# Kernel tuning notes

Measured on AMD Instinct MI355X. Metric: run time of the kernel, lower is better.

The kernel has to match this reference:

```python
import jax, jax.numpy as jnp
import numpy as np

B, T = 16384, 128  # batch, n_frames


def setup_inputs() -> dict:
    key = jax.random.key(0)
    k0, k1, k2, k3, k4, k5 = jax.random.split(key, 6)
    dir = jax.random.normal(k0, (B, 3), dtype=jnp.float32)
    R = jax.random.normal(k1, (B, T, 3, 3), dtype=jnp.float32)
    s = 1.0 / np.sqrt(3.0)  # torch LSTM default init scale (uniform +-1/sqrt(hidden))
    W_ih = jax.random.uniform(k2, (12, 3), jnp.float32, -s, s)
    W_hh = jax.random.uniform(k3, (12, 3), jnp.float32, -s, s)
    b_ih = jax.random.uniform(k4, (12,), jnp.float32, -s, s)
    b_hh = jax.random.uniform(k5, (12,), jnp.float32, -s, s)
    return {"dir": dir, "R": R, "W_ih": W_ih, "W_hh": W_hh, "b_ih": b_ih, "b_hh": b_hh}


def _rot_step(v, Rm):
    # v: [B,3], Rm: [B,3,3] -> Rm @ v
    nv = jnp.einsum('bij,bj->bi', Rm, v)
    return nv, nv


def _build_dirs(dir, R):
    n_frames = R.shape[1]
    half = n_frames // 2
    # Backward chain: dirs[i] = R[half-1-i]^T @ ... @ R[half-1]^T @ dir
    Rt_back = jnp.swapaxes(jnp.flip(R[:, :half], axis=1), 2, 3)  # [B, half, 3, 3]
    _, back = jax.lax.scan(_rot_step, dir, jnp.swapaxes(Rt_back, 0, 1))  # [half, B, 3]
    # Forward chain: dirs[i] = R[i-1] @ ... @ R[half] @ dir for i in half+1..n-1
    Rf = jnp.swapaxes(R[:, half:n_frames - 1], 0, 1)  # [n-1-half, B, 3, 3]
    _, fwd = jax.lax.scan(_rot_step, dir, Rf)  # [n-1-half, B, 3]
    dirs_tm = jnp.concatenate([back, dir[None], fwd], axis=0)  # time-major [T, B, 3]
    return dirs_tm, half


def _lstm(dirs_tm, W_ih, W_hh, b_ih, b_hh):
    Bsz = dirs_tm.shape[1]
    h0 = jnp.zeros((Bsz, 3), dirs_tm.dtype)
    c0 = jnp.zeros((Bsz, 3), dirs_tm.dtype)
    bias = b_ih + b_hh

    def step(carry, x):
        h, c = carry
        gates = x @ W_ih.T + h @ W_hh.T + bias  # [B,12]
        i = jax.nn.sigmoid(gates[:, 0:3])
        f = jax.nn.sigmoid(gates[:, 3:6])
        g = jnp.tanh(gates[:, 6:9])
        o = jax.nn.sigmoid(gates[:, 9:12])
        c = f * c + i * g
        h = o * jnp.tanh(c)
        return (h, c), h

    _, h_seq = jax.lax.scan(step, (h0, c0), dirs_tm)  # [T, B, 3]
    return h_seq


def reference(dir, R, W_ih, W_hh, b_ih, b_hh):
    dirs_tm, half = _build_dirs(dir, R)
    h_seq = _lstm(dirs_tm, W_ih, W_hh, b_ih, b_hh)
    dirs_out = jnp.swapaxes(dirs_tm, 0, 1)  # [B, T, 3]
    return dirs_out.at[:, half, :].set(h_seq[half])
```

## Files before the change

### kernel.cpp

```cpp
#include <hip/hip_runtime.h>

typedef float f4 __attribute__((ext_vector_type(4)));
typedef float f4u __attribute__((ext_vector_type(4), aligned(4)));

struct M3 { float m[3][3]; };

#define ELEM(q, n) ((q)[(n) >> 2][(n) & 3])

__device__ __forceinline__ M3 matmul(const M3& A, const M3& B) {
  M3 C;
#pragma unroll
  for (int i = 0; i < 3; ++i)
#pragma unroll
    for (int j = 0; j < 3; ++j)
      C.m[i][j] = A.m[i][0]*B.m[0][j] + A.m[i][1]*B.m[1][j] + A.m[i][2]*B.m[2][j];
  return C;
}

__device__ __forceinline__ M3 mk18(const f4 (&q)[18], int k) {
  M3 A;
#pragma unroll
  for (int i = 0; i < 3; ++i)
#pragma unroll
    for (int j = 0; j < 3; ++j)
      A.m[i][j] = ELEM(q, 9*k + 3*i + j);
  return A;
}

template <int CTRL>
__device__ __forceinline__ float dppf(float v) {
  return __int_as_float(
      __builtin_amdgcn_mov_dpp(__float_as_int(v), CTRL, 0xf, 0xf, true));
}

template <int D>
__device__ __forceinline__ M3 dpp_shr_mat(const M3& A) {
  M3 C;
#pragma unroll
  for (int i = 0; i < 3; ++i)
#pragma unroll
    for (int j = 0; j < 3; ++j)
      C.m[i][j] = dppf<0x110 + D>(A.m[i][j]);
  return C;
}

__device__ __forceinline__ float sigm(float z) {
  return __builtin_amdgcn_rcpf(1.0f + __expf(-z));
}
__device__ __forceinline__ float tanh_(float z) {
  float e = __expf(2.0f * z);
  return 1.0f - 2.0f * __builtin_amdgcn_rcpf(e + 1.0f);
}

template <int CTRL>
__device__ __forceinline__ float quad_bcast(float v) {
  return __int_as_float(
      __builtin_amdgcn_mov_dpp(__float_as_int(v), CTRL, 0xf, 0xf, true));
}

__global__ __launch_bounds__(64, 2) void fused_kernel(
    const float* __restrict__ dir, const float* __restrict__ R,
    const float* __restrict__ Wih, const float* __restrict__ Whh,
    const float* __restrict__ bih, const float* __restrict__ bhh,
    float* __restrict__ out, int B) {
  __shared__ __align__(16) f4 xrows[64 * 9];

  const int lane = threadIdx.x;
  const int e = lane >> 3;
  const int s = lane & 7;
  const int b0 = blockIdx.x * 8;
  const int b = b0 + e;
  const bool valid = (b < B);
  const int bc = valid ? b : (B - 1);
  const f4* Rb4 = (const f4*)(R + (size_t)bc * 1152);

  f4 q[18], qf[18];
  {
    const f4* pb = Rb4 + 18 * (7 - s);
    const f4* pf = Rb4 + 144 + 18 * s;
#pragma unroll
    for (int i = 0; i < 18; ++i) q[i] = pb[i];
#pragma unroll
    for (int i = 0; i < 18; ++i) qf[i] = pf[i];
  }
  const float d0 = dir[3*bc+0], d1 = dir[3*bc+1], d2 = dir[3*bc+2];

  {
    M3 P = mk18(q, 0);
#pragma unroll
    for (int k = 1; k < 8; ++k) P = matmul(mk18(q, k), P);

    M3 I = P;
    {
      M3 Sh = dpp_shr_mat<1>(I); M3 T = matmul(Sh, I);
#pragma unroll
      for (int i = 0; i < 3; ++i)
#pragma unroll
        for (int j = 0; j < 3; ++j) I.m[i][j] = (s >= 1) ? T.m[i][j] : I.m[i][j];
    }
    {
      M3 Sh = dpp_shr_mat<2>(I); M3 T = matmul(Sh, I);
#pragma unroll
      for (int i = 0; i < 3; ++i)
#pragma unroll
        for (int j = 0; j < 3; ++j) I.m[i][j] = (s >= 2) ? T.m[i][j] : I.m[i][j];
    }
    {
      M3 Sh = dpp_shr_mat<4>(I); M3 T = matmul(Sh, I);
#pragma unroll
      for (int i = 0; i < 3; ++i)
#pragma unroll
        for (int j = 0; j < 3; ++j) I.m[i][j] = (s >= 4) ? T.m[i][j] : I.m[i][j];
    }

    float w0 = I.m[0][0]*d0 + I.m[1][0]*d1 + I.m[2][0]*d2;
    float w1 = I.m[0][1]*d0 + I.m[1][1]*d1 + I.m[2][1]*d2;
    float w2 = I.m[0][2]*d0 + I.m[1][2]*d1 + I.m[2][2]*d2;
    float p0 = dppf<0x111>(w0), p1 = dppf<0x111>(w1), p2 = dppf<0x111>(w2);
    float v0 = (s == 0) ? d0 : p0;
    float v1 = (s == 0) ? d1 : p1;
    float v2 = (s == 0) ? d2 : p2;

    float row[24];
#pragma unroll
    for (int j = 0; j < 8; ++j) {
      M3 A = mk18(q, 7 - j);
      float n0 = v0*A.m[0][0] + v1*A.m[1][0] + v2*A.m[2][0];
      float n1 = v0*A.m[0][1] + v1*A.m[1][1] + v2*A.m[2][1];
      float n2 = v0*A.m[0][2] + v1*A.m[1][2] + v2*A.m[2][2];
      v0 = n0; v1 = n1; v2 = n2;
      row[3*j+0] = n0; row[3*j+1] = n1; row[3*j+2] = n2;
    }

    if (valid) {
      float* ob = out + (size_t)b * 384 + 24 * s;
#pragma unroll
      for (int kk = 0; kk < 6; ++kk) {
        f4 vv = { row[4*kk+0], row[4*kk+1], row[4*kk+2], row[4*kk+3] };
        ((f4*)ob)[kk] = vv;
      }
    }
#pragma unroll
    for (int j = 0; j < 8; ++j) {
      f4 vv = { row[3*j+0], row[3*j+1], row[3*j+2], 0.f };
      xrows[(8*s + j) * 9 + e] = vv;
    }
  }

  {
    M3 P = mk18(qf, 0);
#pragma unroll
    for (int k = 1; k < 8; ++k) P = matmul(mk18(qf, k), P);

    M3 I = P;
    {
      M3 Sh = dpp_shr_mat<1>(I); M3 T = matmul(I, Sh);
#pragma unroll
      for (int i = 0; i < 3; ++i)
#pragma unroll
        for (int j = 0; j < 3; ++j) I.m[i][j] = (s >= 1) ? T.m[i][j] : I.m[i][j];
    }
    {
      M3 Sh = dpp_shr_mat<2>(I); M3 T = matmul(I, Sh);
#pragma unroll
      for (int i = 0; i < 3; ++i)
#pragma unroll
        for (int j = 0; j < 3; ++j) I.m[i][j] = (s >= 2) ? T.m[i][j] : I.m[i][j];
    }
    {
      M3 Sh = dpp_shr_mat<4>(I); M3 T = matmul(I, Sh);
#pragma unroll
      for (int i = 0; i < 3; ++i)
#pragma unroll
        for (int j = 0; j < 3; ++j) I.m[i][j] = (s >= 4) ? T.m[i][j] : I.m[i][j];
    }

    float w0 = I.m[0][0]*d0 + I.m[0][1]*d1 + I.m[0][2]*d2;
    float w1 = I.m[1][0]*d0 + I.m[1][1]*d1 + I.m[1][2]*d2;
    float w2 = I.m[2][0]*d0 + I.m[2][1]*d1 + I.m[2][2]*d2;
    float p0 = dppf<0x111>(w0), p1 = dppf<0x111>(w1), p2 = dppf<0x111>(w2);
    float v0 = (s == 0) ? d0 : p0;
    float v1 = (s == 0) ? d1 : p1;
    float v2 = (s == 0) ? d2 : p2;

    float row[24];
#pragma unroll
    for (int j = 0; j < 8; ++j) {
      M3 A = mk18(qf, j);
      float n0 = A.m[0][0]*v0 + A.m[0][1]*v1 + A.m[0][2]*v2;
      float n1 = A.m[1][0]*v0 + A.m[1][1]*v1 + A.m[1][2]*v2;
      float n2 = A.m[2][0]*v0 + A.m[2][1]*v1 + A.m[2][2]*v2;
      v0 = n0; v1 = n1; v2 = n2;
      row[3*j+0] = n0; row[3*j+1] = n1; row[3*j+2] = n2;
    }

    if (valid) {
      float* ob = out + (size_t)b * 384 + (size_t)(65 + 8*s) * 3;
#pragma unroll
      for (int kk = 0; kk < 5; ++kk) {
        f4u vv = { row[4*kk+0], row[4*kk+1], row[4*kk+2], row[4*kk+3] };
        *(f4u*)(ob + 4*kk) = vv;
      }
      ob[20] = row[20];
      if (s < 7) { ob[21] = row[21]; ob[22] = row[22]; ob[23] = row[23]; }
    }
  }

  if (lane >= 32) return;
  const int e2 = lane >> 2;
  const int u = lane & 3, uu = (u == 3) ? 0 : u;
  const int b2 = b0 + e2;
  const bool valid2 = (b2 < B);
  const int b2c = valid2 ? b2 : 0;

  const float wii0 = Wih[uu*3+0],     wii1 = Wih[uu*3+1],     wii2 = Wih[uu*3+2];
  const float wif0 = Wih[(3+uu)*3+0], wif1 = Wih[(3+uu)*3+1], wif2 = Wih[(3+uu)*3+2];
  const float wig0 = Wih[(6+uu)*3+0], wig1 = Wih[(6+uu)*3+1], wig2 = Wih[(6+uu)*3+2];
  const float wio0 = Wih[(9+uu)*3+0], wio1 = Wih[(9+uu)*3+1], wio2 = Wih[(9+uu)*3+2];
  const float whi0 = Whh[uu*3+0],     whi1 = Whh[uu*3+1],     whi2 = Whh[uu*3+2];
  const float whf0 = Whh[(3+uu)*3+0], whf1 = Whh[(3+uu)*3+1], whf2 = Whh[(3+uu)*3+2];
  const float whg0 = Whh[(6+uu)*3+0], whg1 = Whh[(6+uu)*3+1], whg2 = Whh[(6+uu)*3+2];
  const float who0 = Whh[(9+uu)*3+0], who1 = Whh[(9+uu)*3+1], who2 = Whh[(9+uu)*3+2];
  const float bsi = bih[uu]   + bhh[uu];
  const float bsf = bih[3+uu] + bhh[3+uu];
  const float bsg = bih[6+uu] + bhh[6+uu];
  const float bso = bih[9+uu] + bhh[9+uu];
  const float dd0 = dir[3*b2c+0], dd1 = dir[3*b2c+1], dd2 = dir[3*b2c+2];

  float h0 = 0.f, h1 = 0.f, h2 = 0.f, cc = 0.f, hl = 0.f;

#define LSTEP(x0_, x1_, x2_)                                                  \
  {                                                                           \
    float zi = bsi + wii0*(x0_) + wii1*(x1_) + wii2*(x2_)                     \
                   + whi0*h0 + whi1*h1 + whi2*h2;                             \
    float zf = bsf + wif0*(x0_) + wif1*(x1_) + wif2*(x2_)                     \
                   + whf0*h0 + whf1*h1 + whf2*h2;                             \
    float zg = bsg + wig0*(x0_) + wig1*(x1_) + wig2*(x2_)                     \
                   + whg0*h0 + whg1*h1 + whg2*h2;                             \
    float zo = bso + wio0*(x0_) + wio1*(x1_) + wio2*(x2_)                     \
                   + who0*h0 + who1*h1 + who2*h2;                             \
    float ai = sigm(zi), af = sigm(zf), ag = tanh_(zg), ao = sigm(zo);        \
    cc = af*cc + ai*ag;                                                       \
    float hn = ao * tanh_(cc);                                                \
    hl = hn;                                                                  \
    h0 = quad_bcast<0x00>(hn);                                                \
    h1 = quad_bcast<0x55>(hn);                                                \
    h2 = quad_bcast<0xAA>(hn);                                                \
  }

  f4 xa[8], xb[8];
#pragma unroll
  for (int j = 0; j < 8; ++j) xa[j] = xrows[j * 9 + e2];
#pragma unroll
  for (int c = 0; c < 8; ++c) {
    if (c < 7) {
      if ((c & 1) == 0) {
#pragma unroll
        for (int j = 0; j < 8; ++j) xb[j] = xrows[((c+1)*8 + j) * 9 + e2];
      } else {
#pragma unroll
        for (int j = 0; j < 8; ++j) xa[j] = xrows[((c+1)*8 + j) * 9 + e2];
      }
    }
#pragma unroll
    for (int j = 0; j < 8; ++j) {
      f4 x = ((c & 1) == 0) ? xa[j] : xb[j];
      LSTEP(x[0], x[1], x[2]);
    }
  }
  LSTEP(dd0, dd1, dd2);
#undef LSTEP

  if (valid2 && u < 3) out[(size_t)b2 * 384 + 192 + u] = hl;
}

extern "C" void kernel_launch(void* const* d_in, const int* in_sizes, int n_in,
                              void* d_out, int out_size, void* d_ws, size_t ws_size,
                              hipStream_t stream) {
  const float* dir = (const float*)d_in[0];
  const float* R   = (const float*)d_in[1];
  const float* Wih = (const float*)d_in[2];
  const float* Whh = (const float*)d_in[3];
  const float* bih = (const float*)d_in[4];
  const float* bhh = (const float*)d_in[5];
  float* out = (float*)d_out;

  const int B = in_sizes[0] / 3;
  const int grid = (B + 7) / 8;
  hipLaunchKernelGGL(fused_kernel, dim3(grid), dim3(64), 0, stream,
                     dir, R, Wih, Whh, bih, bhh, out, B);
}
```

Before: 37.89 us.

## Process 16 batch rows per 128-thread block with one full-wave LSTM pass

The block grows to two waves covering 16 batch elements. Both waves compute the rotation chains, then a barrier follows, and the first wave runs the LSTM recurrence for all 16 elements with all 64 lanes active instead of 32. The shared staging buffer is widened to stride 16, the LSTM input loads become a non-unrolled chunk loop without double-buffering, and empty asm statements pin the R loads early. This raises lane utilization in the serial LSTM phase, but the second wave sits idle during it and the loads of the x rows are no longer prefetched.

```diff
diff --git a/kernel.cpp b/kernel.cpp
--- a/kernel.cpp
+++ b/kernel.cpp
@@ -58,17 +58,18 @@
       __builtin_amdgcn_mov_dpp(__float_as_int(v), CTRL, 0xf, 0xf, true));
 }
 
-__global__ __launch_bounds__(64, 2) void fused_kernel(
+__global__ __launch_bounds__(128, 2) void fused_kernel(
     const float* __restrict__ dir, const float* __restrict__ R,
     const float* __restrict__ Wih, const float* __restrict__ Whh,
     const float* __restrict__ bih, const float* __restrict__ bhh,
     float* __restrict__ out, int B) {
-  __shared__ __align__(16) f4 xrows[64 * 9];
-
-  const int lane = threadIdx.x;
-  const int e = lane >> 3;
-  const int s = lane & 7;
-  const int b0 = blockIdx.x * 8;
+  __shared__ __align__(16) f4 xrows[64 * 16];
+
+  const int tid = threadIdx.x;
+  const int lane = tid & 63;
+  const int e = tid >> 3;
+  const int s = tid & 7;
+  const int b0 = blockIdx.x * 16;
   const int b = b0 + e;
   const bool valid = (b < B);
   const int bc = valid ? b : (B - 1);
@@ -83,6 +84,11 @@
 #pragma unroll
     for (int i = 0; i < 18; ++i) qf[i] = pf[i];
   }
+#pragma unroll
+  for (int i = 0; i < 18; ++i) asm volatile("" :: "v"(q[i]));
+#pragma unroll
+  for (int i = 0; i < 18; ++i) asm volatile("" :: "v"(qf[i]));
+
   const float d0 = dir[3*bc+0], d1 = dir[3*bc+1], d2 = dir[3*bc+2];
 
   {
@@ -143,7 +149,7 @@
 #pragma unroll
     for (int j = 0; j < 8; ++j) {
       f4 vv = { row[3*j+0], row[3*j+1], row[3*j+2], 0.f };
-      xrows[(8*s + j) * 9 + e] = vv;
+      xrows[(8*s + j) * 16 + e] = vv;
     }
   }
 
@@ -206,7 +212,9 @@
     }
   }
 
-  if (lane >= 32) return;
+  __syncthreads();
+  if (tid >= 64) return;
+
   const int e2 = lane >> 2;
   const int u = lane & 3, uu = (u == 3) ? 0 : u;
   const int b2 = b0 + e2;
@@ -248,25 +256,13 @@
     h2 = quad_bcast<0xAA>(hn);                                                \
   }
 
-  f4 xa[8], xb[8];
-#pragma unroll
-  for (int j = 0; j < 8; ++j) xa[j] = xrows[j * 9 + e2];
-#pragma unroll
+#pragma unroll 1
   for (int c = 0; c < 8; ++c) {
-    if (c < 7) {
-      if ((c & 1) == 0) {
-#pragma unroll
-        for (int j = 0; j < 8; ++j) xb[j] = xrows[((c+1)*8 + j) * 9 + e2];
-      } else {
-#pragma unroll
-        for (int j = 0; j < 8; ++j) xa[j] = xrows[((c+1)*8 + j) * 9 + e2];
-      }
-    }
-#pragma unroll
-    for (int j = 0; j < 8; ++j) {
-      f4 x = ((c & 1) == 0) ? xa[j] : xb[j];
-      LSTEP(x[0], x[1], x[2]);
-    }
+    f4 xa[8];
+#pragma unroll
+    for (int j = 0; j < 8; ++j) xa[j] = xrows[(c * 8 + j) * 16 + e2];
+#pragma unroll
+    for (int j = 0; j < 8; ++j) LSTEP(xa[j][0], xa[j][1], xa[j][2]);
   }
   LSTEP(dd0, dd1, dd2);
 #undef LSTEP
@@ -286,7 +282,7 @@
   float* out = (float*)d_out;
 
   const int B = in_sizes[0] / 3;
-  const int grid = (B + 7) / 8;
-  hipLaunchKernelGGL(fused_kernel, dim3(grid), dim3(64), 0, stream,
+  const int grid = (B + 15) / 16;
+  hipLaunchKernelGGL(fused_kernel, dim3(grid), dim3(128), 0, stream,
                      dir, R, Wih, Whh, bih, bhh, out, B);
 }
```

Measured after the change: 42.65 us. 12.6% more time.
